# Optimization experiments

Hardware: AMD Instinct MI355X
Metric: run time of the kernel (lower is better)

The kernel has to match this reference:

```python
import jax, jax.numpy as jnp
import numpy as np

N_NODES = 100000
N_EDGES = 600000
N_GRAPHS = 256
K = 5
N_FEAT = 16
N_CLASSES = 4


def setup_inputs() -> dict:
    key = jax.random.key(0)
    ks = jax.random.split(key, 12)
    x = jax.random.normal(ks[0], (N_NODES, N_FEAT), dtype=jnp.float32)
    edge_index = jax.random.randint(ks[1], (2, N_EDGES), 0, N_NODES, dtype=jnp.int32)
    batch = jnp.sort(jax.random.randint(ks[2], (N_NODES,), 0, N_GRAPHS, dtype=jnp.int32))
    s = 0.1
    W11 = jax.random.normal(ks[3], (K, N_FEAT, 64), dtype=jnp.float32) * s
    b11 = jnp.zeros((64,), dtype=jnp.float32)
    W12 = jax.random.normal(ks[4], (K, N_FEAT, 64), dtype=jnp.float32) * s
    b12 = jnp.zeros((64,), dtype=jnp.float32)
    W21 = jax.random.normal(ks[5], (K, 128, 256), dtype=jnp.float32) * s
    b21 = jnp.zeros((256,), dtype=jnp.float32)
    W22 = jax.random.normal(ks[6], (K, 128, 256), dtype=jnp.float32) * s
    b22 = jnp.zeros((256,), dtype=jnp.float32)
    fc_w = jax.random.normal(ks[7], (512, N_CLASSES), dtype=jnp.float32) * s
    fc_b = jnp.zeros((N_CLASSES,), dtype=jnp.float32)
    return {
        "x": x, "edge_index": edge_index, "batch": batch,
        "W11": W11, "b11": b11, "W12": W12, "b12": b12,
        "W21": W21, "b21": b21, "W22": W22, "b22": b22,
        "fc_w": fc_w, "fc_b": fc_b,
    }


def _cheb_norm(src, dst, n_nodes):
    # PyG ChebConv (sym norm, lambda_max=2): L_hat = -D^{-1/2} A D^{-1/2},
    # zero diagonal. Degree computed over source (row) indices.
    deg = jax.ops.segment_sum(jnp.ones_like(src, dtype=jnp.float32), src,
                              num_segments=n_nodes)
    dinv = jnp.where(deg > 0, jax.lax.rsqrt(jnp.maximum(deg, 1.0)), 0.0)
    return -dinv[src] * dinv[dst]


def _cheb_conv(x, src, dst, w_norm, W, b):
    # Chebyshev recursion: Tx0=x, Tx1=L_hat x, Txk = 2 L_hat Tx_{k-1} - Tx_{k-2}
    n = x.shape[0]

    def spmm(h):  # aggregate messages from src at dst
        return jax.ops.segment_sum(h[src] * w_norm[:, None], dst, num_segments=n)

    Tx0 = x
    Tx1 = spmm(x)
    out = jnp.einsum('nf,fo->no', Tx0, W[0]) + jnp.einsum('nf,fo->no', Tx1, W[1])
    for k in range(2, W.shape[0]):
        Tx2 = 2.0 * spmm(Tx1) - Tx0
        out = out + jnp.einsum('nf,fo->no', Tx2, W[k])
        Tx0, Tx1 = Tx1, Tx2
    return out + b


def reference(x, edge_index, batch, W11, b11, W12, b12, W21, b21, W22, b22,
              fc_w, fc_b):
    src, dst = edge_index[0], edge_index[1]
    w_fwd = _cheb_norm(src, dst, N_NODES)
    w_rev = _cheb_norm(dst, src, N_NODES)  # reversed adjacency

    x1 = jax.nn.relu(_cheb_conv(x, src, dst, w_fwd, W11, b11))
    x2 = jax.nn.relu(_cheb_conv(x, dst, src, w_rev, W12, b12))
    h = jnp.concatenate([x1, x2], axis=1)  # [N, 128]

    x1 = jax.nn.relu(_cheb_conv(h, src, dst, w_fwd, W21, b21))
    x2 = jax.nn.relu(_cheb_conv(h, dst, src, w_rev, W22, b22))
    h = jnp.concatenate([x1, x2], axis=1)  # [N, 512]

    # global mean pool over graphs
    sums = jax.ops.segment_sum(h, batch, num_segments=N_GRAPHS)
    cnt = jax.ops.segment_sum(jnp.ones((h.shape[0],), dtype=h.dtype), batch,
                              num_segments=N_GRAPHS)
    pooled = sums / jnp.maximum(cnt, 1.0)[:, None]  # [G, 512]

    logits = pooled @ fc_w + fc_b
    return jax.nn.log_softmax(logits, axis=1)
```

## Files before the change

### kernel.cpp

```cpp
#include <hip/hip_runtime.h>
#include <stdint.h>

#define NNODES 100000
#define NEDGES 600000
#define NGRAPH 256
#define KCH 5
#define F1 16
#define O1 64
#define F2 128
#define O2 256
#define FT1 (KCH * F1)
#define FT2 (KCH * F2)
#define KSTEPS 20
#define KS1 3
#define LROW 40
#define NXCD 8

typedef unsigned short ushort_t;
typedef __attribute__((ext_vector_type(8))) short bf16x8;
typedef __attribute__((ext_vector_type(4))) float f32x4;

__device__ __forceinline__ float bflo(unsigned int u) {
    union { unsigned int u; float f; } v; v.u = u << 16; return v.f;
}
__device__ __forceinline__ float bfhi(unsigned int u) {
    union { unsigned int u; float f; } v; v.u = u & 0xFFFF0000u; return v.f;
}
__device__ __forceinline__ unsigned int f2bf(float f) {
    union { float f; unsigned int u; } v; v.f = f;
    return (v.u + 0x7FFFu + ((v.u >> 16) & 1u)) >> 16;
}
__device__ __forceinline__ unsigned int pack2(float lo, float hi) {
    return (f2bf(hi) << 16) | f2bf(lo);
}


__global__ void k_count(const int* __restrict__ src, const int* __restrict__ dst,
                        int* __restrict__ cntDst, int* __restrict__ cntSrc, int E) {
    int e = blockIdx.x * 256 + threadIdx.x;
    if (e < E) {
        atomicAdd(&cntDst[dst[e]], 1);
        atomicAdd(&cntSrc[src[e]], 1);
    }
}

__global__ void k_dinv(const int* __restrict__ cntDst, const int* __restrict__ cntSrc,
                       float* __restrict__ dinvF, float* __restrict__ dinvR, int n) {
    int i = blockIdx.x * 256 + threadIdx.x;
    if (i < n) {
        int cs = cntSrc[i], cd = cntDst[i];
        dinvF[i] = cs > 0 ? rsqrtf((float)cs) : 0.f;
        dinvR[i] = cd > 0 ? rsqrtf((float)cd) : 0.f;
    }
}

__global__ void k_scan1m(const int* __restrict__ inF, int* __restrict__ outF,
                         int* __restrict__ bsF,
                         const int* __restrict__ inR, int* __restrict__ outR,
                         int* __restrict__ bsR, int n, int NB) {
    __shared__ int a[512];
    __shared__ int s[256];
    int b = blockIdx.x;
    const int* in; int* out; int* bs; int lb;
    if (b < NB) { in = inF; out = outF; bs = bsF; lb = b; }
    else        { in = inR; out = outR; bs = bsR; lb = b - NB; }
    int t = threadIdx.x;
    int base = lb * 512;
    a[t]       = (base + t < n)       ? in[base + t]       : 0;
    a[t + 256] = (base + t + 256 < n) ? in[base + t + 256] : 0;
    __syncthreads();
    s[t] = a[2 * t] + a[2 * t + 1];
    __syncthreads();
    for (int off = 1; off < 256; off <<= 1) {
        int v = (t >= off) ? s[t - off] : 0;
        __syncthreads();
        s[t] += v;
        __syncthreads();
    }
    int ep = (t > 0) ? s[t - 1] : 0;
    if (base + 2 * t < n)     out[base + 2 * t]     = ep;
    if (base + 2 * t + 1 < n) out[base + 2 * t + 1] = ep + a[2 * t];
    if (t == 255) bs[lb] = s[255];
}

__global__ void k_scan2m(int* __restrict__ bsF, int* __restrict__ bsR, int nb) {
    __shared__ int s[256];
    int* bs = (blockIdx.x == 0) ? bsF : bsR;
    int t = threadIdx.x;
    s[t] = (t < nb) ? bs[t] : 0;
    __syncthreads();
    for (int off = 1; off < 256; off <<= 1) {
        int v = (t >= off) ? s[t - off] : 0;
        __syncthreads();
        s[t] += v;
        __syncthreads();
    }
    if (t < nb) bs[t] = (t > 0) ? s[t - 1] : 0;
}

__global__ void k_scan3m(int* __restrict__ outF, int* __restrict__ curF,
                         const int* __restrict__ bsF,
                         int* __restrict__ outR, int* __restrict__ curR,
                         const int* __restrict__ bsR, int n, int E, int NB) {
    int b = blockIdx.x;
    int* out; int* cur; const int* bs; int lb;
    if (b < NB) { out = outF; cur = curF; bs = bsF; lb = b; }
    else        { out = outR; cur = curR; bs = bsR; lb = b - NB; }
    int i = lb * 512 + threadIdx.x;
    int add = bs[lb];
    if (i < n)       { int v = out[i] + add;       out[i] = v;       cur[i] = v; }
    if (i + 256 < n) { int v = out[i + 256] + add; out[i + 256] = v; cur[i + 256] = v; }
    if (lb == 0 && threadIdx.x == 0) out[n] = E;
}

__global__ void k_scatter(const int* __restrict__ src, const int* __restrict__ dst,
                          const float* __restrict__ dinvF, const float* __restrict__ dinvR,
                          int* __restrict__ curF, int* __restrict__ curR,
                          int2* __restrict__ edF, int2* __restrict__ edR, int E,
                          int chunk) {
    int c = blockIdx.x & (NXCD - 1);
    int sb = blockIdx.x >> 3;
    int slices = gridDim.x >> 3;
    int lo = c * chunk, hi = lo + chunk;
    for (int e = sb * 256 + threadIdx.x; e < E; e += slices * 256) {
        int s = src[e], d = dst[e];
        if (d >= lo && d < hi) {
            int p = atomicAdd(&curF[d], 1);
            float wf = -dinvF[s] * dinvF[d];
            edF[p] = make_int2(s, __float_as_int(wf));
        }
        if (s >= lo && s < hi) {
            int q = atomicAdd(&curR[s], 1);
            float wr = -dinvR[s] * dinvR[d];
            edR[q] = make_int2(d, __float_as_int(wr));
        }
    }
}

__global__ void k_gstart(const int* __restrict__ batch, int* __restrict__ gstart, int n) {
    int g = blockIdx.x * 64 + threadIdx.x;
    if (g > NGRAPH) return;
    if (g == NGRAPH) { gstart[g] = n; return; }
    int lo = 0, hi = n;
    while (lo < hi) {
        int mid = (lo + hi) >> 1;
        if (batch[mid] < g) lo = mid + 1; else hi = mid;
    }
    gstart[g] = lo;
}


__global__ void k_copyx(const float* __restrict__ x, float* __restrict__ Tx,
                        ushort_t* __restrict__ TxB, int n) {
    int tid = blockIdx.x * 256 + threadIdx.x;
    int r = tid >> 2, c = tid & 3;
    if (r < n) {
        float4 v = *(const float4*)(x + (size_t)r * 16 + c * 4);
        *(float4*)(Tx + (size_t)r * FT1 + c * 4) = v;
        uint2 b;
        b.x = pack2(v.x, v.y);
        b.y = pack2(v.z, v.w);
        *(uint2*)(TxB + (size_t)r * F1 + c * 4) = b;
    }
}

__global__ void k_spmm_f32(const ushort_t* __restrict__ HinB, float* __restrict__ Hout,
                           ushort_t* __restrict__ HoutB,
                           const float* __restrict__ Tx0,
                           const int* __restrict__ off, const int2* __restrict__ ed,
                           int n) {
    int tid = blockIdx.x * 256 + threadIdx.x;
    int r = tid >> 2, c = tid & 3;
    if (r >= n) return;
    int j0 = off[r], j1 = off[r + 1];
    float4 s = {0.f, 0.f, 0.f, 0.f};
    int j = j0;
    for (; j + 4 <= j1; j += 4) {
        int2 e0 = ed[j], e1 = ed[j + 1], e2 = ed[j + 2], e3 = ed[j + 3];
        float wa = __int_as_float(e0.y), wb = __int_as_float(e1.y);
        float wc = __int_as_float(e2.y), wd = __int_as_float(e3.y);
        const uint2 h0 = *(const uint2*)(HinB + (size_t)e0.x * F1 + c * 4);
        const uint2 h1 = *(const uint2*)(HinB + (size_t)e1.x * F1 + c * 4);
        const uint2 h2 = *(const uint2*)(HinB + (size_t)e2.x * F1 + c * 4);
        const uint2 h3 = *(const uint2*)(HinB + (size_t)e3.x * F1 + c * 4);
        s.x = fmaf(wa, bflo(h0.x), s.x); s.y = fmaf(wa, bfhi(h0.x), s.y);
        s.z = fmaf(wa, bflo(h0.y), s.z); s.w = fmaf(wa, bfhi(h0.y), s.w);
        s.x = fmaf(wb, bflo(h1.x), s.x); s.y = fmaf(wb, bfhi(h1.x), s.y);
        s.z = fmaf(wb, bflo(h1.y), s.z); s.w = fmaf(wb, bfhi(h1.y), s.w);
        s.x = fmaf(wc, bflo(h2.x), s.x); s.y = fmaf(wc, bfhi(h2.x), s.y);
        s.z = fmaf(wc, bflo(h2.y), s.z); s.w = fmaf(wc, bfhi(h2.y), s.w);
        s.x = fmaf(wd, bflo(h3.x), s.x); s.y = fmaf(wd, bfhi(h3.x), s.y);
        s.z = fmaf(wd, bflo(h3.y), s.z); s.w = fmaf(wd, bfhi(h3.y), s.w);
    }
    for (; j < j1; ++j) {
        int2 e = ed[j];
        float w2 = __int_as_float(e.y);
        const uint2 h = *(const uint2*)(HinB + (size_t)e.x * F1 + c * 4);
        s.x = fmaf(w2, bflo(h.x), s.x); s.y = fmaf(w2, bfhi(h.x), s.y);
        s.z = fmaf(w2, bflo(h.y), s.z); s.w = fmaf(w2, bfhi(h.y), s.w);
    }
    float4 o;
    if (Tx0) {
        const float4 t0 = *(const float4*)(Tx0 + (size_t)r * FT1 + c * 4);
        o.x = 2.f * s.x - t0.x; o.y = 2.f * s.y - t0.y;
        o.z = 2.f * s.z - t0.z; o.w = 2.f * s.w - t0.w;
    } else {
        o = s;
    }
    *(float4*)(Hout + (size_t)r * FT1 + c * 4) = o;
    if (HoutB) {
        uint2 b;
        b.x = pack2(o.x, o.y);
        b.y = pack2(o.z, o.w);
        *(uint2*)(HoutB + (size_t)r * F1 + c * 4) = b;
    }
}

__global__ void k_spmm_bf(const ushort_t* __restrict__ Hin, ushort_t* __restrict__ Hout,
                          const ushort_t* __restrict__ Tx0,
                          const int* __restrict__ off, const int2* __restrict__ ed,
                          int n) {
    int r = blockIdx.x * 4 + (threadIdx.x >> 6);
    r = __builtin_amdgcn_readfirstlane(r);
    int c = threadIdx.x & 63;
    if (r >= n) return;
    int j0 = __builtin_amdgcn_readfirstlane(off[r]);
    int j1 = __builtin_amdgcn_readfirstlane(off[r + 1]);
    float s0 = 0.f, s1 = 0.f;

    auto loadblk = [&](int jb, float* W, unsigned int* H) {
        if (jb + 8 <= j1) {
#pragma unroll
            for (int sl = 0; sl < 8; ++sl) {
                int2 e = ed[jb + sl];
                W[sl] = __int_as_float(e.y);
                H[sl] = *(const unsigned int*)(Hin + (size_t)e.x * FT2 + c * 2);
            }
        } else {
#pragma unroll
            for (int sl = 0; sl < 8; ++sl) {
                W[sl] = 0.f; H[sl] = 0u;
                if (jb + sl < j1) {
                    int2 e = ed[jb + sl];
                    W[sl] = __int_as_float(e.y);
                    H[sl] = *(const unsigned int*)(Hin + (size_t)e.x * FT2 + c * 2);
                }
            }
        }
    };
    auto fmablk = [&](const float* W, const unsigned int* H) {
#pragma unroll
        for (int sl = 0; sl < 8; ++sl) {
            s0 = fmaf(bflo(H[sl]), W[sl], s0);
            s1 = fmaf(bfhi(H[sl]), W[sl], s1);
        }
    };

    float wA[8], wB[8];
    unsigned int hA[8], hB[8];
    if (j0 < j1) {
        loadblk(j0, wA, hA);
        for (int j = j0; j < j1; j += 16) {
            bool hasB = (j + 8 < j1);
            if (hasB) loadblk(j + 8, wB, hB);
            fmablk(wA, hA);
            if (hasB) {
                if (j + 16 < j1) loadblk(j + 16, wA, hA);
                fmablk(wB, hB);
            }
        }
    }
    if (Tx0) {
        unsigned int t0 = *(const unsigned int*)(Tx0 + (size_t)r * FT2 + c * 2);
        s0 = 2.f * s0 - bflo(t0);
        s1 = 2.f * s1 - bfhi(t0);
    }
    *(unsigned int*)(Hout + (size_t)r * FT2 + c * 2) = pack2(s0, s1);
}

__global__ void k_packW1m(const float* __restrict__ WF, ushort_t* __restrict__ BpF_,
                          const float* __restrict__ WR, ushort_t* __restrict__ BpR_) {
    int b = blockIdx.x;
    const float* W = (b < 3) ? WF : WR;
    ushort_t* Bp = (b < 3) ? BpF_ : BpR_;
    int tid = ((b < 3) ? b : b - 3) * 256 + threadIdx.x;
    if (tid >= 4 * KS1 * 64) return;
    int lane = tid & 63;
    int ks = (tid >> 6) % KS1;
    int nt = tid / (64 * KS1);
    int k0 = ks * 32 + (lane >> 4) * 8;
    int ncol = nt * 16 + (lane & 15);
    float v[8];
#pragma unroll
    for (int j = 0; j < 8; ++j) {
        int k = k0 + j;
        v[j] = (k < FT1) ? W[(size_t)k * O1 + ncol] : 0.f;
    }
    uint4 o;
    o.x = pack2(v[0], v[1]); o.y = pack2(v[2], v[3]);
    o.z = pack2(v[4], v[5]); o.w = pack2(v[6], v[7]);
    *(uint4*)(Bp + (size_t)tid * 8) = o;
}

__global__ __launch_bounds__(256) void k_gemm1_mfma(
    const float* __restrict__ A, const ushort_t* __restrict__ Bp,
    const float* __restrict__ bias, ushort_t* __restrict__ out, int n) {
    int lane = threadIdx.x & 63;
    int wvi = threadIdx.x >> 6;
    int mrow = lane & 15;
    int quad = lane >> 4;
    int m0w = blockIdx.x * 64 + wvi * 16;
    int row = m0w + mrow;
    int rowc = row < n ? row : n - 1;
    const float* Ar = A + (size_t)rowc * FT1 + quad * 8;

    f32x4 acc[4] = {};
#pragma unroll
    for (int ks = 0; ks < KS1; ++ks) {
        float4 a0 = *(const float4*)(Ar + ks * 32);
        float4 a1 = *(const float4*)(Ar + ks * 32 + 4);
        union { bf16x8 v; unsigned int u[4]; } ua;
        ua.u[0] = pack2(a0.x, a0.y);
        ua.u[1] = pack2(a0.z, a0.w);
        ua.u[2] = pack2(a1.x, a1.y);
        ua.u[3] = pack2(a1.z, a1.w);
#pragma unroll
        for (int nf = 0; nf < 4; ++nf) {
            bf16x8 bfr = *(const bf16x8*)(Bp + ((size_t)(nf * KS1 + ks) * 64 + lane) * 8);
            acc[nf] = __builtin_amdgcn_mfma_f32_16x16x32_bf16(ua.v, bfr, acc[nf], 0, 0, 0);
        }
    }
#pragma unroll
    for (int nf = 0; nf < 4; ++nf) {
        float bb = bias[nf * 16 + mrow];
#pragma unroll
        for (int reg = 0; reg < 4; ++reg) {
            int orow = m0w + quad * 4 + reg;
            if (orow < n)
                out[(size_t)orow * FT2 + nf * 16 + mrow] =
                    (ushort_t)f2bf(fmaxf(acc[nf][reg] + bb, 0.f));
        }
    }
}

__global__ void k_packWm(const float* __restrict__ WF, ushort_t* __restrict__ BpF_,
                         const float* __restrict__ WR, ushort_t* __restrict__ BpR_) {
    int b = blockIdx.x;
    const float* W = (b < 80) ? WF : WR;
    ushort_t* Bp = (b < 80) ? BpF_ : BpR_;
    int tid = ((b < 80) ? b : b - 80) * 256 + threadIdx.x;
    if (tid >= 16 * KSTEPS * 64) return;
    int lane = tid & 63;
    int ks = (tid >> 6) % KSTEPS;
    int nt = tid / (64 * KSTEPS);
    int k0 = ks * 32 + (lane >> 4) * 8;
    int ncol = nt * 16 + (lane & 15);
    float v[8];
#pragma unroll
    for (int j = 0; j < 8; ++j) v[j] = W[(size_t)(k0 + j) * O2 + ncol];
    uint4 o;
    o.x = pack2(v[0], v[1]); o.y = pack2(v[2], v[3]);
    o.z = pack2(v[4], v[5]); o.w = pack2(v[6], v[7]);
    *(uint4*)(Bp + (size_t)tid * 8) = o;
}

__global__ __launch_bounds__(256, 2) void k_gemm2_mfma(
    const ushort_t* __restrict__ A, const ushort_t* __restrict__ Bp,
    const float* __restrict__ bias, float* __restrict__ pooled, int colofs,
    const int* __restrict__ batch, int n) {
    __shared__ ushort_t lds[2][128 * LROW];

    int lane = threadIdx.x & 63;
    int wv = threadIdx.x >> 6;
    int m0 = blockIdx.x * 128;
    int mrow = lane & 15;
    int quad = lane >> 4;
    int srow = threadIdx.x >> 1;
    int sc = threadIdx.x & 1;

    const ushort_t* Ag = A + (size_t)(m0 + srow) * FT2 + sc * 16;
    const ushort_t* Bbase = Bp + ((size_t)(wv * 4) * KSTEPS * 64 + lane) * 8;
    int sidx = srow * LROW + sc * 16;

    f32x4 acc[8][4] = {};
    uint4 nxt0, nxt1;
    bf16x8 bcur[4], bnxt[4];

    *(uint4*)&lds[0][sidx]     = *(const uint4*)(Ag);
    *(uint4*)&lds[0][sidx + 8] = *(const uint4*)(Ag + 8);
    nxt0 = *(const uint4*)(Ag + 32);
    nxt1 = *(const uint4*)(Ag + 40);
#pragma unroll
    for (int nf = 0; nf < 4; ++nf)
        bcur[nf] = *(const bf16x8*)(Bbase + ((size_t)nf * KSTEPS) * 512);

    for (int ks = 0; ks < KSTEPS; ++ks) {
        __syncthreads();
        if (ks + 1 < KSTEPS) {
            *(uint4*)&lds[(ks + 1) & 1][sidx]     = nxt0;
            *(uint4*)&lds[(ks + 1) & 1][sidx + 8] = nxt1;
        }
        if (ks + 2 < KSTEPS) {
            nxt0 = *(const uint4*)(Ag + (ks + 2) * 32);
            nxt1 = *(const uint4*)(Ag + (ks + 2) * 32 + 8);
        }
        if (ks + 1 < KSTEPS) {
#pragma unroll
            for (int nf = 0; nf < 4; ++nf)
                bnxt[nf] = *(const bf16x8*)(Bbase + ((size_t)nf * KSTEPS + ks + 1) * 512);
        }
        const ushort_t* lbuf = &lds[ks & 1][0];
        bf16x8 af[8];
#pragma unroll
        for (int mf = 0; mf < 8; ++mf)
            af[mf] = *(const bf16x8*)(lbuf + (mf * 16 + mrow) * LROW + quad * 8);
#pragma unroll
        for (int mf = 0; mf < 8; ++mf)
#pragma unroll
            for (int nf = 0; nf < 4; ++nf)
                acc[mf][nf] = __builtin_amdgcn_mfma_f32_16x16x32_bf16(
                    af[mf], bcur[nf], acc[mf][nf], 0, 0, 0);
#pragma unroll
        for (int nf = 0; nf < 4; ++nf) bcur[nf] = bnxt[nf];
    }

    float bcol[4];
#pragma unroll
    for (int nf = 0; nf < 4; ++nf) bcol[nf] = bias[wv * 64 + nf * 16 + mrow];

#pragma unroll
    for (int mf = 0; mf < 8; ++mf) {
        int t0 = m0 + mf * 16;
        if (t0 >= n) break;
        int te = (t0 + 15 < n) ? t0 + 15 : n - 1;
        int r0 = t0 + quad * 4;
        if (batch[t0] == batch[te]) {
            int g = batch[t0];
#pragma unroll
            for (int nf = 0; nf < 4; ++nf) {
                float s = 0.f;
#pragma unroll
                for (int reg = 0; reg < 4; ++reg) {
                    float v = fmaxf(acc[mf][nf][reg] + bcol[nf], 0.f);
                    if (r0 + reg < n) s += v;
                }
                s += __shfl_xor(s, 16, 64);
                s += __shfl_xor(s, 32, 64);
                if (quad == 0)
                    atomicAdd(pooled + (size_t)g * 512 + colofs + wv * 64 + nf * 16 + mrow, s);
            }
        } else {
            int gb[4];
#pragma unroll
            for (int reg = 0; reg < 4; ++reg)
                gb[reg] = batch[(r0 + reg < n) ? r0 + reg : n - 1];
#pragma unroll
            for (int nf = 0; nf < 4; ++nf) {
                int col = colofs + wv * 64 + nf * 16 + mrow;
                float run = 0.f;
                int g = gb[0];
                bool any = false;
#pragma unroll
                for (int reg = 0; reg < 4; ++reg) {
                    int row = r0 + reg;
                    if (row >= n) break;
                    float v = fmaxf(acc[mf][nf][reg] + bcol[nf], 0.f);
                    if (gb[reg] != g) {
                        atomicAdd(pooled + (size_t)g * 512 + col, run);
                        run = 0.f;
                        g = gb[reg];
                    }
                    run += v;
                    any = true;
                }
                if (any) atomicAdd(pooled + (size_t)g * 512 + col, run);
            }
        }
    }
}

__global__ void k_logits(const float* __restrict__ pooled, const int* __restrict__ gstart,
                         const float* __restrict__ fcw, const float* __restrict__ fcb,
                         float* __restrict__ out) {
    int g = threadIdx.x;
    int cnt = gstart[g + 1] - gstart[g];
    float inv = 1.f / (float)(cnt > 1 ? cnt : 1);
    float lg[4];
#pragma unroll
    for (int o = 0; o < 4; ++o) lg[o] = fcb[o];
    for (int f = 0; f < 512; ++f) {
        float p = pooled[g * 512 + f] * inv;
#pragma unroll
        for (int o = 0; o < 4; ++o) lg[o] = fmaf(p, fcw[f * 4 + o], lg[o]);
    }
    float m = fmaxf(fmaxf(lg[0], lg[1]), fmaxf(lg[2], lg[3]));
    float s = 0.f;
#pragma unroll
    for (int o = 0; o < 4; ++o) s += expf(lg[o] - m);
    float l = logf(s);
#pragma unroll
    for (int o = 0; o < 4; ++o) out[g * 4 + o] = lg[o] - m - l;
}


extern "C" void kernel_launch(void* const* d_in, const int* in_sizes, int n_in,
                              void* d_out, int out_size, void* d_ws, size_t ws_size,
                              hipStream_t stream) {
    const float* x   = (const float*)d_in[0];
    const int* ei    = (const int*)d_in[1];
    const int* batch = (const int*)d_in[2];
    const float* W11 = (const float*)d_in[3];
    const float* b11 = (const float*)d_in[4];
    const float* W12 = (const float*)d_in[5];
    const float* b12 = (const float*)d_in[6];
    const float* W21 = (const float*)d_in[7];
    const float* b21 = (const float*)d_in[8];
    const float* W22 = (const float*)d_in[9];
    const float* b22 = (const float*)d_in[10];
    const float* fcw = (const float*)d_in[11];
    const float* fcb = (const float*)d_in[12];
    float* out = (float*)d_out;

    const int N = in_sizes[0] / F1;
    const int E = in_sizes[1] / 2;
    const int* src = ei;
    const int* dst = ei + E;

    char* w = (char*)d_ws;
    size_t pos = 0;
    auto alloc = [&](size_t bytes) -> void* {
        void* p = w + pos;
        pos += (bytes + 255) & ~(size_t)255;
        return p;
    };
    int* cur_f   = (int*)alloc((size_t)N * 4);
    int* cur_r   = (int*)alloc((size_t)N * 4);
    int* off_f   = (int*)alloc((size_t)(N + 1) * 4);
    int* off_r   = (int*)alloc((size_t)(N + 1) * 4);
    float* dinvF = (float*)alloc((size_t)N * 4);
    float* dinvR = (float*)alloc((size_t)N * 4);
    int2* ed_f   = (int2*)alloc((size_t)E * 8);
    int2* ed_r   = (int2*)alloc((size_t)E * 8);
    int* blks_f  = (int*)alloc(1024);
    int* blks_r  = (int*)alloc(1024);
    int* gstart  = (int*)alloc((NGRAPH + 1) * 4);
    float* pooled = (float*)alloc((size_t)NGRAPH * 512 * 4);
    ushort_t* BpF = (ushort_t*)alloc((size_t)FT2 * O2 * 2);
    ushort_t* BpR = (ushort_t*)alloc((size_t)FT2 * O2 * 2);
    ushort_t* Bp1F = (ushort_t*)alloc((size_t)4 * KS1 * 64 * 8 * 2);
    ushort_t* Bp1R = (ushort_t*)alloc((size_t)4 * KS1 * 64 * 8 * 2);
    float* TxAll1 = (float*)alloc(((size_t)N * FT1 + 256) * 4);
    ushort_t* TxB1 = (ushort_t*)alloc((size_t)KCH * N * F1 * 2);
    ushort_t* TxAll2 = (ushort_t*)alloc((size_t)(N + 128) * FT2 * 2);

    (void)hipMemsetAsync(cur_f, 0, (size_t)N * 4, stream);
    (void)hipMemsetAsync(cur_r, 0, (size_t)N * 4, stream);
    (void)hipMemsetAsync(pooled, 0, (size_t)NGRAPH * 512 * 4, stream);

    int gE = (E + 255) / 256, gN = (N + 255) / 256;
    k_count<<<gE, 256, 0, stream>>>(src, dst, cur_f, cur_r, E);
    k_dinv<<<gN, 256, 0, stream>>>(cur_f, cur_r, dinvF, dinvR, N);

    int NB = (N + 511) / 512;
    k_scan1m<<<2 * NB, 256, 0, stream>>>(cur_f, off_f, blks_f, cur_r, off_r, blks_r, N, NB);
    k_scan2m<<<2, 256, 0, stream>>>(blks_f, blks_r, NB);
    k_scan3m<<<2 * NB, 256, 0, stream>>>(off_f, cur_f, blks_f, off_r, cur_r, blks_r, N, E, NB);
    int chunk = (N + NXCD - 1) / NXCD;
    k_scatter<<<NXCD * 256, 256, 0, stream>>>(src, dst, dinvF, dinvR, cur_f, cur_r,
                                              ed_f, ed_r, E, chunk);
    k_gstart<<<5, 64, 0, stream>>>(batch, gstart, N);
    k_packWm<<<160, 256, 0, stream>>>(W21, BpF, W22, BpR);
    k_packW1m<<<6, 256, 0, stream>>>(W11, Bp1F, W12, Bp1R);

    k_copyx<<<(N * 4 + 255) / 256, 256, 0, stream>>>(x, TxAll1, TxB1, N);
    int gs1 = (N * 4 + 255) / 256;
    int gg1 = (N + 63) / 64;
    auto C1 = [&](int k) { return TxAll1 + k * F1; };
    auto B1 = [&](int k) { return TxB1 + (size_t)k * N * F1; };
    k_spmm_f32<<<gs1, 256, 0, stream>>>(B1(0), C1(1), B1(1), nullptr, off_f, ed_f, N);
    k_spmm_f32<<<gs1, 256, 0, stream>>>(B1(1), C1(2), B1(2), C1(0), off_f, ed_f, N);
    k_spmm_f32<<<gs1, 256, 0, stream>>>(B1(2), C1(3), B1(3), C1(1), off_f, ed_f, N);
    k_spmm_f32<<<gs1, 256, 0, stream>>>(B1(3), C1(4), nullptr, C1(2), off_f, ed_f, N);
    k_gemm1_mfma<<<gg1, 256, 0, stream>>>(TxAll1, Bp1F, b11, TxAll2, N);
    k_spmm_f32<<<gs1, 256, 0, stream>>>(B1(0), C1(1), B1(1), nullptr, off_r, ed_r, N);
    k_spmm_f32<<<gs1, 256, 0, stream>>>(B1(1), C1(2), B1(2), C1(0), off_r, ed_r, N);
    k_spmm_f32<<<gs1, 256, 0, stream>>>(B1(2), C1(3), B1(3), C1(1), off_r, ed_r, N);
    k_spmm_f32<<<gs1, 256, 0, stream>>>(B1(3), C1(4), nullptr, C1(2), off_r, ed_r, N);
    k_gemm1_mfma<<<gg1, 256, 0, stream>>>(TxAll1, Bp1R, b12, TxAll2 + O1, N);

    int gs2 = (N + 3) / 4;
    auto C2 = [&](int k) { return TxAll2 + k * F2; };
    int gg = (N + 127) / 128;
    k_spmm_bf<<<gs2, 256, 0, stream>>>(C2(0), C2(1), nullptr, off_f, ed_f, N);
    k_spmm_bf<<<gs2, 256, 0, stream>>>(C2(1), C2(2), C2(0), off_f, ed_f, N);
    k_spmm_bf<<<gs2, 256, 0, stream>>>(C2(2), C2(3), C2(1), off_f, ed_f, N);
    k_spmm_bf<<<gs2, 256, 0, stream>>>(C2(3), C2(4), C2(2), off_f, ed_f, N);
    k_gemm2_mfma<<<gg, 256, 0, stream>>>(TxAll2, BpF, b21, pooled, 0, batch, N);
    k_spmm_bf<<<gs2, 256, 0, stream>>>(C2(0), C2(1), nullptr, off_r, ed_r, N);
    k_spmm_bf<<<gs2, 256, 0, stream>>>(C2(1), C2(2), C2(0), off_r, ed_r, N);
    k_spmm_bf<<<gs2, 256, 0, stream>>>(C2(2), C2(3), C2(1), off_r, ed_r, N);
    k_spmm_bf<<<gs2, 256, 0, stream>>>(C2(3), C2(4), C2(2), off_r, ed_r, N);
    k_gemm2_mfma<<<gg, 256, 0, stream>>>(TxAll2, BpR, b22, pooled, 256, batch, N);

    k_logits<<<1, 256, 0, stream>>>(pooled, gstart, fcw, fcb, out);
}
```

Before: 792.3 us.

## Fuse last Chebyshev SpMM step into layer-2 GEMM and shrink TxAll2 stride

The fourth SpMM of each layer-2 Chebyshev recursion is now computed inside the GEMM kernel. Results go to LDS and feed the last four K-steps directly, so Tx4 is never written to or re-read from global memory. The GEMM tile shrinks from 128 to 64 rows, TxAll2's row stride drops from 640 to 512 since Tx4 is no longer stored, and the standalone SpMM loses its double-buffered software pipeline. The logits kernel is parallelised to one block per graph with a wave reduction, in exchange for fewer MFMA tiles per block and a serial gather phase ahead of the GEMM.

```diff
diff --git a/kernel.cpp b/kernel.cpp
--- a/kernel.cpp
+++ b/kernel.cpp
@@ -11,9 +11,11 @@
 #define O2 256
 #define FT1 (KCH * F1)
 #define FT2 (KCH * F2)
+#define STR2 512
 #define KSTEPS 20
 #define KS1 3
 #define LROW 40
+#define LROWD 68
 #define NXCD 8
 
 typedef unsigned short ushort_t;
@@ -227,55 +229,48 @@
     int j0 = __builtin_amdgcn_readfirstlane(off[r]);
     int j1 = __builtin_amdgcn_readfirstlane(off[r + 1]);
     float s0 = 0.f, s1 = 0.f;
-
-    auto loadblk = [&](int jb, float* W, unsigned int* H) {
-        if (jb + 8 <= j1) {
-#pragma unroll
-            for (int sl = 0; sl < 8; ++sl) {
-                int2 e = ed[jb + sl];
-                W[sl] = __int_as_float(e.y);
-                H[sl] = *(const unsigned int*)(Hin + (size_t)e.x * FT2 + c * 2);
+    int j = j0;
+    int jfull = j0 + ((j1 - j0) & ~7);
+    for (; j < jfull; j += 8) {
+        float w[8];
+        unsigned int h[8];
+#pragma unroll
+        for (int sl = 0; sl < 8; ++sl) {
+            int2 e = ed[j + sl];
+            w[sl] = __int_as_float(e.y);
+            h[sl] = *(const unsigned int*)(Hin + (size_t)e.x * STR2 + c * 2);
+        }
+#pragma unroll
+        for (int sl = 0; sl < 8; ++sl) {
+            s0 = fmaf(bflo(h[sl]), w[sl], s0);
+            s1 = fmaf(bfhi(h[sl]), w[sl], s1);
+        }
+    }
+    int rem = j1 - j;
+    if (rem) {
+        float w[8];
+        unsigned int h[8];
+#pragma unroll
+        for (int sl = 0; sl < 8; ++sl) {
+            w[sl] = 0.f; h[sl] = 0u;
+            if (sl < rem) {
+                int2 e = ed[j + sl];
+                w[sl] = __int_as_float(e.y);
+                h[sl] = *(const unsigned int*)(Hin + (size_t)e.x * STR2 + c * 2);
             }
-        } else {
-#pragma unroll
-            for (int sl = 0; sl < 8; ++sl) {
-                W[sl] = 0.f; H[sl] = 0u;
-                if (jb + sl < j1) {
-                    int2 e = ed[jb + sl];
-                    W[sl] = __int_as_float(e.y);
-                    H[sl] = *(const unsigned int*)(Hin + (size_t)e.x * FT2 + c * 2);
-                }
-            }
-        }
-    };
-    auto fmablk = [&](const float* W, const unsigned int* H) {
+        }
 #pragma unroll
         for (int sl = 0; sl < 8; ++sl) {
-            s0 = fmaf(bflo(H[sl]), W[sl], s0);
-            s1 = fmaf(bfhi(H[sl]), W[sl], s1);
-        }
-    };
-
-    float wA[8], wB[8];
-    unsigned int hA[8], hB[8];
-    if (j0 < j1) {
-        loadblk(j0, wA, hA);
-        for (int j = j0; j < j1; j += 16) {
-            bool hasB = (j + 8 < j1);
-            if (hasB) loadblk(j + 8, wB, hB);
-            fmablk(wA, hA);
-            if (hasB) {
-                if (j + 16 < j1) loadblk(j + 16, wA, hA);
-                fmablk(wB, hB);
-            }
+            s0 = fmaf(bflo(h[sl]), w[sl], s0);
+            s1 = fmaf(bfhi(h[sl]), w[sl], s1);
         }
     }
     if (Tx0) {
-        unsigned int t0 = *(const unsigned int*)(Tx0 + (size_t)r * FT2 + c * 2);
+        unsigned int t0 = *(const unsigned int*)(Tx0 + (size_t)r * STR2 + c * 2);
         s0 = 2.f * s0 - bflo(t0);
         s1 = 2.f * s1 - bfhi(t0);
     }
-    *(unsigned int*)(Hout + (size_t)r * FT2 + c * 2) = pack2(s0, s1);
+    *(unsigned int*)(Hout + (size_t)r * STR2 + c * 2) = pack2(s0, s1);
 }
 
 __global__ void k_packW1m(const float* __restrict__ WF, ushort_t* __restrict__ BpF_,
@@ -337,7 +332,7 @@
         for (int reg = 0; reg < 4; ++reg) {
             int orow = m0w + quad * 4 + reg;
             if (orow < n)
-                out[(size_t)orow * FT2 + nf * 16 + mrow] =
+                out[(size_t)orow * STR2 + nf * 16 + mrow] =
                     (ushort_t)f2bf(fmaxf(acc[nf][reg] + bb, 0.f));
         }
     }
@@ -364,58 +359,118 @@
     *(uint4*)(Bp + (size_t)tid * 8) = o;
 }
 
-__global__ __launch_bounds__(256, 2) void k_gemm2_mfma(
-    const ushort_t* __restrict__ A, const ushort_t* __restrict__ Bp,
+__global__ __launch_bounds__(256) void k_spmm4_gemm(
+    const ushort_t* __restrict__ Hin,
+    const ushort_t* __restrict__ Txc,
+    const int* __restrict__ off, const int2* __restrict__ ed,
+    const ushort_t* __restrict__ A,
+    const ushort_t* __restrict__ Bp,
     const float* __restrict__ bias, float* __restrict__ pooled, int colofs,
     const int* __restrict__ batch, int n) {
-    __shared__ ushort_t lds[2][128 * LROW];
+    __shared__ ushort_t lds[2][64 * LROW];
+    __shared__ unsigned int a4[64 * LROWD];
 
     int lane = threadIdx.x & 63;
     int wv = threadIdx.x >> 6;
-    int m0 = blockIdx.x * 128;
+    int m0 = blockIdx.x * 64;
+
+    for (int i = 0; i < 16; ++i) {
+        int r = m0 + wv * 16 + i;
+        float s0 = 0.f, s1 = 0.f;
+        if (r < n) {
+            int j0 = __builtin_amdgcn_readfirstlane(off[r]);
+            int j1 = __builtin_amdgcn_readfirstlane(off[r + 1]);
+            int j = j0;
+            int jfull = j0 + ((j1 - j0) & ~7);
+            for (; j < jfull; j += 8) {
+                float w[8];
+                unsigned int h[8];
+#pragma unroll
+                for (int sl = 0; sl < 8; ++sl) {
+                    int2 e = ed[j + sl];
+                    w[sl] = __int_as_float(e.y);
+                    h[sl] = *(const unsigned int*)(Hin + (size_t)e.x * STR2 + lane * 2);
+                }
+#pragma unroll
+                for (int sl = 0; sl < 8; ++sl) {
+                    s0 = fmaf(bflo(h[sl]), w[sl], s0);
+                    s1 = fmaf(bfhi(h[sl]), w[sl], s1);
+                }
+            }
+            int rem = j1 - j;
+            if (rem) {
+                float w[8];
+                unsigned int h[8];
+#pragma unroll
+                for (int sl = 0; sl < 8; ++sl) {
+                    w[sl] = 0.f; h[sl] = 0u;
+                    if (sl < rem) {
+                        int2 e = ed[j + sl];
+                        w[sl] = __int_as_float(e.y);
+                        h[sl] = *(const unsigned int*)(Hin + (size_t)e.x * STR2 + lane * 2);
+                    }
+                }
+#pragma unroll
+                for (int sl = 0; sl < 8; ++sl) {
+                    s0 = fmaf(bflo(h[sl]), w[sl], s0);
+                    s1 = fmaf(bfhi(h[sl]), w[sl], s1);
+                }
+            }
+            unsigned int t0 = *(const unsigned int*)(Txc + (size_t)r * STR2 + lane * 2);
+            s0 = 2.f * s0 - bflo(t0);
+            s1 = 2.f * s1 - bfhi(t0);
+        }
+        a4[(wv * 16 + i) * LROWD + lane] = pack2(s0, s1);
+    }
+    __syncthreads();
+
     int mrow = lane & 15;
     int quad = lane >> 4;
-    int srow = threadIdx.x >> 1;
-    int sc = threadIdx.x & 1;
-
-    const ushort_t* Ag = A + (size_t)(m0 + srow) * FT2 + sc * 16;
+    int srow = threadIdx.x >> 2;
+    int sc = threadIdx.x & 3;
+
+    const ushort_t* Ag = A + (size_t)(m0 + srow) * STR2 + sc * 8;
     const ushort_t* Bbase = Bp + ((size_t)(wv * 4) * KSTEPS * 64 + lane) * 8;
-    int sidx = srow * LROW + sc * 16;
-
-    f32x4 acc[8][4] = {};
-    uint4 nxt0, nxt1;
+    int sidx = srow * LROW + sc * 8;
+
+    f32x4 acc[4][4] = {};
+    uint4 nxt;
     bf16x8 bcur[4], bnxt[4];
-
-    *(uint4*)&lds[0][sidx]     = *(const uint4*)(Ag);
-    *(uint4*)&lds[0][sidx + 8] = *(const uint4*)(Ag + 8);
-    nxt0 = *(const uint4*)(Ag + 32);
-    nxt1 = *(const uint4*)(Ag + 40);
-#pragma unroll
-    for (int nf = 0; nf < 4; ++nf)
-        bcur[nf] = *(const bf16x8*)(Bbase + ((size_t)nf * KSTEPS) * 512);
+    {
+        uint4 c0 = *(const uint4*)(Ag);
+        *(uint4*)&lds[0][sidx] = c0;
+        nxt = *(const uint4*)(Ag + 32);
+#pragma unroll
+        for (int nf = 0; nf < 4; ++nf)
+            bcur[nf] = *(const bf16x8*)(Bbase + ((size_t)nf * KSTEPS) * 512);
+    }
 
     for (int ks = 0; ks < KSTEPS; ++ks) {
         __syncthreads();
-        if (ks + 1 < KSTEPS) {
-            *(uint4*)&lds[(ks + 1) & 1][sidx]     = nxt0;
-            *(uint4*)&lds[(ks + 1) & 1][sidx + 8] = nxt1;
-        }
-        if (ks + 2 < KSTEPS) {
-            nxt0 = *(const uint4*)(Ag + (ks + 2) * 32);
-            nxt1 = *(const uint4*)(Ag + (ks + 2) * 32 + 8);
-        }
+        if (ks + 1 < 16)
+            *(uint4*)&lds[(ks + 1) & 1][sidx] = nxt;
+        if (ks + 2 < 16)
+            nxt = *(const uint4*)(Ag + (ks + 2) * 32);
         if (ks + 1 < KSTEPS) {
 #pragma unroll
             for (int nf = 0; nf < 4; ++nf)
                 bnxt[nf] = *(const bf16x8*)(Bbase + ((size_t)nf * KSTEPS + ks + 1) * 512);
         }
-        const ushort_t* lbuf = &lds[ks & 1][0];
-        bf16x8 af[8];
-#pragma unroll
-        for (int mf = 0; mf < 8; ++mf)
-            af[mf] = *(const bf16x8*)(lbuf + (mf * 16 + mrow) * LROW + quad * 8);
-#pragma unroll
-        for (int mf = 0; mf < 8; ++mf)
+        bf16x8 af[4];
+        if (ks < 16) {
+            const ushort_t* lbuf = &lds[ks & 1][0];
+#pragma unroll
+            for (int mf = 0; mf < 4; ++mf)
+                af[mf] = *(const bf16x8*)(lbuf + (mf * 16 + mrow) * LROW + quad * 8);
+        } else {
+            int kk = ks - 16;
+#pragma unroll
+            for (int mf = 0; mf < 4; ++mf)
+                af[mf] = *(const bf16x8*)(a4 + (size_t)(mf * 16 + mrow) * LROWD +
+                                          kk * 16 + quad * 4);
+        }
+#pragma unroll
+        for (int mf = 0; mf < 4; ++mf)
 #pragma unroll
             for (int nf = 0; nf < 4; ++nf)
                 acc[mf][nf] = __builtin_amdgcn_mfma_f32_16x16x32_bf16(
@@ -429,7 +484,7 @@
     for (int nf = 0; nf < 4; ++nf) bcol[nf] = bias[wv * 64 + nf * 16 + mrow];
 
 #pragma unroll
-    for (int mf = 0; mf < 8; ++mf) {
+    for (int mf = 0; mf < 4; ++mf) {
         int t0 = m0 + mf * 16;
         if (t0 >= n) break;
         int te = (t0 + 15 < n) ? t0 + 15 : n - 1;
@@ -482,24 +537,36 @@
 __global__ void k_logits(const float* __restrict__ pooled, const int* __restrict__ gstart,
                          const float* __restrict__ fcw, const float* __restrict__ fcb,
                          float* __restrict__ out) {
-    int g = threadIdx.x;
+    int g = blockIdx.x;
+    int l = threadIdx.x;
     int cnt = gstart[g + 1] - gstart[g];
     float inv = 1.f / (float)(cnt > 1 ? cnt : 1);
-    float lg[4];
-#pragma unroll
-    for (int o = 0; o < 4; ++o) lg[o] = fcb[o];
-    for (int f = 0; f < 512; ++f) {
+    float lg0 = 0.f, lg1 = 0.f, lg2 = 0.f, lg3 = 0.f;
+    for (int f = l; f < 512; f += 64) {
         float p = pooled[g * 512 + f] * inv;
-#pragma unroll
-        for (int o = 0; o < 4; ++o) lg[o] = fmaf(p, fcw[f * 4 + o], lg[o]);
-    }
-    float m = fmaxf(fmaxf(lg[0], lg[1]), fmaxf(lg[2], lg[3]));
-    float s = 0.f;
-#pragma unroll
-    for (int o = 0; o < 4; ++o) s += expf(lg[o] - m);
-    float l = logf(s);
-#pragma unroll
-    for (int o = 0; o < 4; ++o) out[g * 4 + o] = lg[o] - m - l;
+        const float4 wv4 = *(const float4*)(fcw + f * 4);
+        lg0 = fmaf(p, wv4.x, lg0);
+        lg1 = fmaf(p, wv4.y, lg1);
+        lg2 = fmaf(p, wv4.z, lg2);
+        lg3 = fmaf(p, wv4.w, lg3);
+    }
+#pragma unroll
+    for (int o = 32; o > 0; o >>= 1) {
+        lg0 += __shfl_down(lg0, o, 64);
+        lg1 += __shfl_down(lg1, o, 64);
+        lg2 += __shfl_down(lg2, o, 64);
+        lg3 += __shfl_down(lg3, o, 64);
+    }
+    if (l == 0) {
+        float lg[4] = {lg0 + fcb[0], lg1 + fcb[1], lg2 + fcb[2], lg3 + fcb[3]};
+        float m = fmaxf(fmaxf(lg[0], lg[1]), fmaxf(lg[2], lg[3]));
+        float s = 0.f;
+#pragma unroll
+        for (int o = 0; o < 4; ++o) s += expf(lg[o] - m);
+        float lsum = logf(s);
+#pragma unroll
+        for (int o = 0; o < 4; ++o) out[g * 4 + o] = lg[o] - m - lsum;
+    }
 }
 
 
@@ -551,7 +618,7 @@
     ushort_t* Bp1R = (ushort_t*)alloc((size_t)4 * KS1 * 64 * 8 * 2);
     float* TxAll1 = (float*)alloc(((size_t)N * FT1 + 256) * 4);
     ushort_t* TxB1 = (ushort_t*)alloc((size_t)KCH * N * F1 * 2);
-    ushort_t* TxAll2 = (ushort_t*)alloc((size_t)(N + 128) * FT2 * 2);
+    ushort_t* TxAll2 = (ushort_t*)alloc((size_t)(N + 64) * STR2 * 2);
 
     (void)hipMemsetAsync(cur_f, 0, (size_t)N * 4, stream);
     (void)hipMemsetAsync(cur_r, 0, (size_t)N * 4, stream);
@@ -590,17 +657,17 @@
 
     int gs2 = (N + 3) / 4;
     auto C2 = [&](int k) { return TxAll2 + k * F2; };
-    int gg = (N + 127) / 128;
+    int gg = (N + 63) / 64;
     k_spmm_bf<<<gs2, 256, 0, stream>>>(C2(0), C2(1), nullptr, off_f, ed_f, N);
     k_spmm_bf<<<gs2, 256, 0, stream>>>(C2(1), C2(2), C2(0), off_f, ed_f, N);
     k_spmm_bf<<<gs2, 256, 0, stream>>>(C2(2), C2(3), C2(1), off_f, ed_f, N);
-    k_spmm_bf<<<gs2, 256, 0, stream>>>(C2(3), C2(4), C2(2), off_f, ed_f, N);
-    k_gemm2_mfma<<<gg, 256, 0, stream>>>(TxAll2, BpF, b21, pooled, 0, batch, N);
+    k_spmm4_gemm<<<gg, 256, 0, stream>>>(C2(3), C2(2), off_f, ed_f, TxAll2, BpF,
+                                         b21, pooled, 0, batch, N);
     k_spmm_bf<<<gs2, 256, 0, stream>>>(C2(0), C2(1), nullptr, off_r, ed_r, N);
     k_spmm_bf<<<gs2, 256, 0, stream>>>(C2(1), C2(2), C2(0), off_r, ed_r, N);
     k_spmm_bf<<<gs2, 256, 0, stream>>>(C2(2), C2(3), C2(1), off_r, ed_r, N);
-    k_spmm_bf<<<gs2, 256, 0, stream>>>(C2(3), C2(4), C2(2), off_r, ed_r, N);
-    k_gemm2_mfma<<<gg, 256, 0, stream>>>(TxAll2, BpR, b22, pooled, 256, batch, N);
-
-    k_logits<<<1, 256, 0, stream>>>(pooled, gstart, fcw, fcb, out);
-}
+    k_spmm4_gemm<<<gg, 256, 0, stream>>>(C2(3), C2(2), off_r, ed_r, TxAll2, BpR,
+                                         b22, pooled, 256, batch, N);
+
+    k_logits<<<NGRAPH, 64, 0, stream>>>(pooled, gstart, fcw, fcb, out);
+}
```

New measurement: 854.8 us. 7.9% more time.
